# Kernel tuning notes

Measured on AMD Instinct MI355X. Metric: run time of the kernel, lower is better.

The kernel has to match this reference:

```python
import jax, jax.numpy as jnp
import numpy as np

B, S, HID = 2, 2048, 2048
H, KV, D = 16, 4, 128
EPS = 1e-6


def rms_norm(x, w, eps=EPS):
    # Qwen3.5 convention: (1 + weight) * RMSNorm(x), weight init 0
    v = jnp.mean(x * x, axis=-1, keepdims=True)
    return (1.0 + w) * (x * jax.lax.rsqrt(v + eps))


def rotate_half(x):
    x1, x2 = jnp.split(x, 2, axis=-1)
    return jnp.concatenate([-x2, x1], axis=-1)


def apply_rope(x, cos, sin):
    # x: [B,S,h,D]; cos/sin: [S,D]
    c = cos[None, :, None, :]
    s = sin[None, :, None, :]
    return x * c + rotate_half(x) * s


def setup_inputs():
    key = jax.random.key(0)
    ks = jax.random.split(key, 8)
    sc = 0.02
    hidden_states = jax.random.normal(ks[0], (B, S, HID), jnp.float32)
    past_key_value = jnp.zeros((B, 2, KV, S, D), jnp.float32)
    pos = jnp.arange(S, dtype=jnp.float32)
    inv_freq = 1.0 / (10000.0 ** (jnp.arange(0, D, 2, dtype=jnp.float32) / D))
    ang = pos[:, None] * inv_freq[None, :]                    # [S, D/2]
    cos = jnp.concatenate([jnp.cos(ang), jnp.cos(ang)], -1)   # [S, D]
    sin = jnp.concatenate([jnp.sin(ang), jnp.sin(ang)], -1)
    rope_rotary_cos_sin = jnp.stack([cos, sin], axis=1)       # [S, 2, D]
    context_lengths = jnp.full((B,), S, dtype=jnp.int32)
    kvcache_start_index = jnp.zeros((B,), dtype=jnp.int32)
    Wq = jax.random.normal(ks[1], (HID, H * D * 2), jnp.float32) * sc
    Wk = jax.random.normal(ks[2], (HID, KV * D), jnp.float32) * sc
    Wv = jax.random.normal(ks[3], (HID, KV * D), jnp.float32) * sc
    Wo = jax.random.normal(ks[4], (H * D, HID), jnp.float32) * sc
    q_norm_w = jax.random.normal(ks[5], (D,), jnp.float32) * sc
    k_norm_w = jax.random.normal(ks[6], (D,), jnp.float32) * sc
    return {"hidden_states": hidden_states, "past_key_value": past_key_value,
            "rope_rotary_cos_sin": rope_rotary_cos_sin,
            "context_lengths": context_lengths,
            "kvcache_start_index": kvcache_start_index,
            "Wq": Wq, "Wk": Wk, "Wv": Wv, "Wo": Wo,
            "q_norm_w": q_norm_w, "k_norm_w": k_norm_w}


def reference(hidden_states, past_key_value, rope_rotary_cos_sin,
              context_lengths, kvcache_start_index,
              Wq, Wk, Wv, Wo, q_norm_w, k_norm_w):
    # projections
    q_out = jnp.einsum('bsc,cd->bsd', hidden_states, Wq).reshape(B, S, H, 2 * D)
    query, gate = jnp.split(q_out, 2, axis=-1)                # each [B,S,H,D]
    k = jnp.einsum('bsc,cd->bsd', hidden_states, Wk).reshape(B, S, KV, D)
    v = jnp.einsum('bsc,cd->bsd', hidden_states, Wv).reshape(B, S, KV, D)
    # per-head QK RMSNorm
    query = rms_norm(query, q_norm_w)
    k = rms_norm(k, k_norm_w)
    # RoPE
    cos, sin = rope_rotary_cos_sin[:, 0, :], rope_rotary_cos_sin[:, 1, :]
    query = apply_rope(query, cos, sin)
    k = apply_rope(k, cos, sin)
    # write KV cache (prefill at start index 0)
    present = past_key_value.at[:, 0, :, :S, :].set(jnp.transpose(k, (0, 2, 1, 3)))
    present = present.at[:, 1, :, :S, :].set(jnp.transpose(v, (0, 2, 1, 3)))
    # GQA causal attention
    group = H // KV
    k_r = jnp.repeat(k, group, axis=2)                        # [B,S,H,D]
    v_r = jnp.repeat(v, group, axis=2)
    scores = jnp.einsum('bqhd,bkhd->bhqk', query, k_r) / jnp.sqrt(jnp.float32(D))
    causal = jnp.tril(jnp.ones((S, S), dtype=bool))
    scores = jnp.where(causal[None, None], scores, jnp.float32(-1e30))
    probs = jax.nn.softmax(scores, axis=-1)
    attn = jnp.einsum('bhqk,bkhd->bqhd', probs, v_r)          # [B,S,H,D]
    # sigmoid gating + output proj
    attn = attn * jax.nn.sigmoid(gate)
    out = jnp.einsum('bsd,dc->bsc', attn.reshape(B, S, H * D), Wo)
    return out, present
```

## Files before the change

kernel.cpp:

```cpp
#include <hip/hip_runtime.h>
#include <hip/hip_bf16.h>
#include <cstdint>
#include <cstddef>

#define BB   2
#define SS   2048
#define HIDD 2048
#define HH   16
#define KVH  4
#define DD   128
#define NQKV 5120
#define MM   4096

typedef unsigned short u16t;
typedef __attribute__((ext_vector_type(8))) short s16x8;
typedef __attribute__((ext_vector_type(4))) short s16x4;
typedef __attribute__((ext_vector_type(4))) float f32x4;

__device__ __forceinline__ u16t f2bf(float f) {
  unsigned u = __float_as_uint(f);
  u += 0x7fffu + ((u >> 16) & 1u);
  return (u16t)(u >> 16);
}
__device__ __forceinline__ float bf2f(u16t h) {
  return __uint_as_float(((unsigned)h) << 16);
}
__device__ __forceinline__ void gload_lds16(const void* g, void* l) {
  __builtin_amdgcn_global_load_lds(
      (const __attribute__((address_space(1))) unsigned int*)g,
      (__attribute__((address_space(3))) unsigned int*)l, 16, 0, 0);
}
__device__ __forceinline__ unsigned cvtpk_bf16(float lo, float hi) {
  unsigned r;
  asm("v_cvt_pk_bf16_f32 %0, %1, %2" : "=v"(r) : "v"(lo), "v"(hi));
  return r;
}
__device__ __forceinline__ f32x4 fmax4(f32x4 a, f32x4 b) {
  f32x4 r;
  r[0] = fmaxf(a[0], b[0]); r[1] = fmaxf(a[1], b[1]);
  r[2] = fmaxf(a[2], b[2]); r[3] = fmaxf(a[3], b[3]);
  return r;
}

__global__ __launch_bounds__(256) void cast_x(const float* __restrict__ in,
                                              u16t* __restrict__ out) {
  size_t i = ((size_t)blockIdx.x * 256 + threadIdx.x) * 4;
  f32x4 v = *(const f32x4*)(in + i);
  s16x4 o;
  o[0] = (short)f2bf(v[0]); o[1] = (short)f2bf(v[1]);
  o[2] = (short)f2bf(v[2]); o[3] = (short)f2bf(v[3]);
  *(s16x4*)(out + i) = o;
}

__global__ __launch_bounds__(256) void transpose_cast(const float* __restrict__ src,
                                                      u16t* __restrict__ dst, int N) {
  __shared__ float lds[64 * 65];
  int t = threadIdx.x;
  const int ktiles = HIDD / 64;
  int n0 = (blockIdx.x / ktiles) << 6;
  int k0 = (blockIdx.x % ktiles) << 6;
#pragma unroll
  for (int i = 0; i < 16; i++) {
    int idx = i * 256 + t;
    int r = idx >> 6, c = idx & 63;
    lds[c * 65 + r] = src[(size_t)(k0 + r) * N + n0 + c];
  }
  __syncthreads();
#pragma unroll
  for (int i = 0; i < 16; i++) {
    int idx = i * 256 + t;
    int rr = idx >> 6, kk = idx & 63;
    dst[(size_t)(n0 + rr) * HIDD + k0 + kk] = f2bf(lds[rr * 65 + kk]);
  }
}

__device__ __forceinline__ s16x8 ldsfrag(const char* half, int r, int g) {
  return *(const s16x8*)(half + r * 64 + ((g ^ ((r >> 1) & 3)) << 4));
}
__device__ __forceinline__ void stage_half(char* ldsbase, const u16t* gbase,
                                           int K, int kcol, int tid) {
#pragma unroll
  for (int i = 0; i < 2; i++) {
    int o16 = i * 512 + tid;
    int r = o16 >> 2;
    int cs = (o16 & 3) ^ ((r >> 1) & 3);
    gload_lds16(gbase + (size_t)r * K + kcol + cs * 8, ldsbase + o16 * 16);
  }
}

template <typename CT>
__global__ __launch_bounds__(512, 2) void gemm8(const u16t* __restrict__ A,
                                                const u16t* __restrict__ Bt,
                                                CT* __restrict__ C,
                                                int M, int N, int K) {
  extern __shared__ __align__(16) char lds[];
  char* As = lds;
  char* Bs = lds + 65536;
  int tid = threadIdx.x, lane = tid & 63, w = tid >> 6;
  int wm = w >> 2, wn = w & 3;
  int cpx = gridDim.x >> 3;
  int wgid = (blockIdx.x & 7) * cpx + (blockIdx.x >> 3);
  int bm = wgid & 15, bn = wgid >> 4;
  int m0 = bm << 8, n0 = bn << 8;
  const u16t* Ag = A + (size_t)m0 * K;
  const u16t* Bg = Bt + (size_t)n0 * K;
  const int NT = K >> 6;

  stage_half(As, Ag, K, 0, tid);
  stage_half(Bs, Bg, K, 0, tid);
  stage_half(As + 16384, Ag, K, 32, tid);
  stage_half(Bs + 16384, Bg, K, 32, tid);
  stage_half(As + 32768, Ag, K, 64, tid);
  stage_half(Bs + 32768, Bg, K, 64, tid);
  asm volatile("s_waitcnt vmcnt(8)" ::: "memory");
  __builtin_amdgcn_s_barrier();

  const f32x4 fz = {0.f, 0.f, 0.f, 0.f};
  f32x4 acc[8][4];
#pragma unroll
  for (int i = 0; i < 8; i++)
#pragma unroll
    for (int j = 0; j < 4; j++) acc[i][j] = fz;
  s16x8 afr[4], bfr[4];
  int g = lane >> 4;
  int rA = (lane & 15) + wm * 128;
  int rB = (lane & 15) + wn * 64;

  for (int kt = 0; kt < NT; kt++) {
    int cur = kt & 1;
    char* Acur = As + cur * 32768;
    char* Bcur = Bs + cur * 32768;
    char* Anxt = As + (cur ^ 1) * 32768;
    char* Bnxt = Bs + (cur ^ 1) * 32768;
#pragma unroll
    for (int ni = 0; ni < 4; ni++) bfr[ni] = ldsfrag(Bcur, rB + ni * 16, g);
#pragma unroll
    for (int mi = 0; mi < 4; mi++) afr[mi] = ldsfrag(Acur, rA + mi * 16, g);
    if (kt + 1 < NT) stage_half(Anxt + 16384, Ag, K, (kt + 1) * 64 + 32, tid);
    __builtin_amdgcn_s_barrier();
    asm volatile("s_waitcnt lgkmcnt(0)" ::: "memory");
    __builtin_amdgcn_s_setprio(1);
#pragma unroll
    for (int mi = 0; mi < 4; mi++)
#pragma unroll
      for (int ni = 0; ni < 4; ni++)
        acc[mi][ni] = __builtin_amdgcn_mfma_f32_16x16x32_bf16(afr[mi], bfr[ni], acc[mi][ni], 0, 0, 0);
    __builtin_amdgcn_s_setprio(0);
    __builtin_amdgcn_s_barrier();
#pragma unroll
    for (int mi = 0; mi < 4; mi++) afr[mi] = ldsfrag(Acur, rA + 64 + mi * 16, g);
    if (kt + 1 < NT) stage_half(Bnxt + 16384, Bg, K, (kt + 1) * 64 + 32, tid);
    __builtin_amdgcn_s_barrier();
    asm volatile("s_waitcnt lgkmcnt(0)" ::: "memory");
    __builtin_amdgcn_s_setprio(1);
#pragma unroll
    for (int mi = 0; mi < 4; mi++)
#pragma unroll
      for (int ni = 0; ni < 4; ni++)
        acc[4 + mi][ni] = __builtin_amdgcn_mfma_f32_16x16x32_bf16(afr[mi], bfr[ni], acc[4 + mi][ni], 0, 0, 0);
    __builtin_amdgcn_s_setprio(0);
    if (kt + 1 < NT) asm volatile("s_waitcnt vmcnt(8)" ::: "memory");
    else             asm volatile("s_waitcnt vmcnt(0)" ::: "memory");
    __builtin_amdgcn_s_barrier();
#pragma unroll
    for (int ni = 0; ni < 4; ni++) bfr[ni] = ldsfrag(Bcur + 16384, rB + ni * 16, g);
#pragma unroll
    for (int mi = 0; mi < 4; mi++) afr[mi] = ldsfrag(Acur + 16384, rA + mi * 16, g);
    if (kt + 2 < NT) stage_half(Acur, Ag, K, (kt + 2) * 64, tid);
    __builtin_amdgcn_s_barrier();
    asm volatile("s_waitcnt lgkmcnt(0)" ::: "memory");
    __builtin_amdgcn_s_setprio(1);
#pragma unroll
    for (int mi = 0; mi < 4; mi++)
#pragma unroll
      for (int ni = 0; ni < 4; ni++)
        acc[mi][ni] = __builtin_amdgcn_mfma_f32_16x16x32_bf16(afr[mi], bfr[ni], acc[mi][ni], 0, 0, 0);
    __builtin_amdgcn_s_setprio(0);
    __builtin_amdgcn_s_barrier();
#pragma unroll
    for (int mi = 0; mi < 4; mi++) afr[mi] = ldsfrag(Acur + 16384, rA + 64 + mi * 16, g);
    if (kt + 2 < NT) stage_half(Bcur, Bg, K, (kt + 2) * 64, tid);
    __builtin_amdgcn_s_barrier();
    asm volatile("s_waitcnt lgkmcnt(0)" ::: "memory");
    __builtin_amdgcn_s_setprio(1);
#pragma unroll
    for (int mi = 0; mi < 4; mi++)
#pragma unroll
      for (int ni = 0; ni < 4; ni++)
        acc[4 + mi][ni] = __builtin_amdgcn_mfma_f32_16x16x32_bf16(afr[mi], bfr[ni], acc[4 + mi][ni], 0, 0, 0);
    __builtin_amdgcn_s_setprio(0);
    if (kt < NT - 1) {
      if (kt + 2 < NT) asm volatile("s_waitcnt vmcnt(8)" ::: "memory");
      else             asm volatile("s_waitcnt vmcnt(4)" ::: "memory");
    }
    __builtin_amdgcn_s_barrier();
  }
#pragma unroll
  for (int mi = 0; mi < 8; mi++)
#pragma unroll
    for (int ni = 0; ni < 4; ni++) {
      int row0 = m0 + wm * 128 + mi * 16 + ((lane >> 4) << 2);
      int col = n0 + wn * 64 + ni * 16 + (lane & 15);
#pragma unroll
      for (int j = 0; j < 4; j++) {
        if constexpr (sizeof(CT) == 2)
          C[(size_t)(row0 + j) * N + col] = f2bf(acc[mi][ni][j]);
        else
          C[(size_t)(row0 + j) * N + col] = acc[mi][ni][j];
      }
    }
}

template <typename CT>
__global__ __launch_bounds__(256) void gemm_bt(const u16t* __restrict__ A,
                                               const u16t* __restrict__ Bt,
                                               CT* __restrict__ C,
                                               int M, int N, int K) {
  __shared__ __align__(16) char As[128 * 64];
  __shared__ __align__(16) char Bs[128 * 64];
  int tid = threadIdx.x;
  int lane = tid & 63;
  int w = tid >> 6;
  int cpx = gridDim.x >> 3;
  int wgid = ((int)blockIdx.x & 7) * cpx + ((int)blockIdx.x >> 3);
  int mtiles = M >> 7;
  int bm = wgid % mtiles;
  int bn = wgid / mtiles;
  int m0 = bm << 7, n0 = bn << 7;
  int wr = (w >> 1) * 64, wc = (w & 1) * 64;

  const f32x4 fz = {0.f, 0.f, 0.f, 0.f};
  f32x4 acc[4][4];
#pragma unroll
  for (int i = 0; i < 4; i++)
#pragma unroll
    for (int j = 0; j < 4; j++) acc[i][j] = fz;

  for (int k0 = 0; k0 < K; k0 += 32) {
    __syncthreads();
#pragma unroll
    for (int i = 0; i < 2; i++) {
      int idx = i * 256 + tid;
      int r = idx >> 2, c = idx & 3;
      int csrc = c ^ ((r >> 1) & 3);
      gload_lds16(A + (size_t)(m0 + r) * K + k0 + csrc * 8, As + idx * 16);
      gload_lds16(Bt + (size_t)(n0 + r) * K + k0 + csrc * 8, Bs + idx * 16);
    }
    __syncthreads();
    s16x8 af[4], bf[4];
    int g = lane >> 4;
#pragma unroll
    for (int mi = 0; mi < 4; mi++) {
      int r = wr + mi * 16 + (lane & 15);
      af[mi] = *(const s16x8*)(As + r * 64 + ((g ^ ((r >> 1) & 3)) << 4));
    }
#pragma unroll
    for (int ni = 0; ni < 4; ni++) {
      int r = wc + ni * 16 + (lane & 15);
      bf[ni] = *(const s16x8*)(Bs + r * 64 + ((g ^ ((r >> 1) & 3)) << 4));
    }
#pragma unroll
    for (int mi = 0; mi < 4; mi++)
#pragma unroll
      for (int ni = 0; ni < 4; ni++)
        acc[mi][ni] = __builtin_amdgcn_mfma_f32_16x16x32_bf16(af[mi], bf[ni], acc[mi][ni], 0, 0, 0);
  }
#pragma unroll
  for (int mi = 0; mi < 4; mi++)
#pragma unroll
    for (int ni = 0; ni < 4; ni++) {
      int row0 = m0 + wr + mi * 16 + ((lane >> 4) << 2);
      int col = n0 + wc + ni * 16 + (lane & 15);
#pragma unroll
      for (int j = 0; j < 4; j++) {
        if constexpr (sizeof(CT) == 2)
          C[(size_t)(row0 + j) * N + col] = f2bf(acc[mi][ni][j]);
        else
          C[(size_t)(row0 + j) * N + col] = acc[mi][ni][j];
      }
    }
}

__global__ __launch_bounds__(256) void qk_norm_rope(const u16t* __restrict__ Cqkv,
                                                    const float* __restrict__ rope,
                                                    const float* __restrict__ qw,
                                                    const float* __restrict__ kw,
                                                    u16t* __restrict__ Qb,
                                                    u16t* __restrict__ Kb,
                                                    u16t* __restrict__ Gs,
                                                    float* __restrict__ present) {
  int wid = blockIdx.x * 4 + (threadIdx.x >> 6);
  int lane = threadIdx.x & 63;
  const int NQ = BB * SS * HH;
  if (wid < NQ) {
    int b = wid >> 15;
    int rem = wid & 32767;
    int s = rem >> 4, h = rem & 15;
    const u16t* base = Cqkv + (size_t)(b * SS + s) * NQKV + h * 256;
    float xlo = bf2f(base[lane]), xhi = bf2f(base[64 + lane]);
    float ss = xlo * xlo + xhi * xhi;
    ss += __shfl_xor(ss, 1);  ss += __shfl_xor(ss, 2);  ss += __shfl_xor(ss, 4);
    ss += __shfl_xor(ss, 8);  ss += __shfl_xor(ss, 16); ss += __shfl_xor(ss, 32);
    float r = rsqrtf(ss * (1.f / 128.f) + 1e-6f);
    float qlo = xlo * r * (1.f + qw[lane]);
    float qhi = xhi * r * (1.f + qw[64 + lane]);
    const float* cs = rope + (size_t)s * 256;
    float clo = cs[lane], chi = cs[64 + lane];
    float slo = cs[128 + lane], shi = cs[192 + lane];
    const float SC = 0.08838834764831845f * 1.4426950408889634f;
    float olo = (qlo * clo - qhi * slo) * SC;
    float ohi = (qhi * chi + qlo * shi) * SC;
    size_t qoff = (((size_t)b * HH + h) * SS + s) * DD;
    Qb[qoff + lane] = f2bf(olo);
    Qb[qoff + 64 + lane] = f2bf(ohi);
    float glo = bf2f(base[128 + lane]), ghi = bf2f(base[192 + lane]);
    size_t goff = ((size_t)(b * SS + s)) * (HH * DD) + h * DD;
    Gs[goff + lane] = f2bf(1.f / (1.f + __expf(-glo)));
    Gs[goff + 64 + lane] = f2bf(1.f / (1.f + __expf(-ghi)));
  } else {
    int wid2 = wid - NQ;
    int b = wid2 >> 13;
    int rem = wid2 & 8191;
    int s = rem >> 2, kv = rem & 3;
    const u16t* base = Cqkv + (size_t)(b * SS + s) * NQKV + 4096 + kv * 128;
    float xlo = bf2f(base[lane]), xhi = bf2f(base[64 + lane]);
    float ss = xlo * xlo + xhi * xhi;
    ss += __shfl_xor(ss, 1);  ss += __shfl_xor(ss, 2);  ss += __shfl_xor(ss, 4);
    ss += __shfl_xor(ss, 8);  ss += __shfl_xor(ss, 16); ss += __shfl_xor(ss, 32);
    float r = rsqrtf(ss * (1.f / 128.f) + 1e-6f);
    float klo = xlo * r * (1.f + kw[lane]);
    float khi = xhi * r * (1.f + kw[64 + lane]);
    const float* cs = rope + (size_t)s * 256;
    float clo = cs[lane], chi = cs[64 + lane];
    float slo = cs[128 + lane], shi = cs[192 + lane];
    float olo = klo * clo - khi * slo;
    float ohi = khi * chi + klo * shi;
    size_t koff = (((size_t)b * KVH + kv) * SS + s) * DD;
    Kb[koff + lane] = f2bf(olo);
    Kb[koff + 64 + lane] = f2bf(ohi);
    size_t poff = (((size_t)(b * 2 * KVH + kv)) * SS + s) * DD;
    present[poff + lane] = olo;
    present[poff + 64 + lane] = ohi;
  }
}

__global__ __launch_bounds__(256) void v_write(const u16t* __restrict__ Cqkv,
                                               float* __restrict__ present,
                                               u16t* __restrict__ Vtb) {
  __shared__ float lds[128 * 65];
  int t = threadIdx.x;
  int b = blockIdx.x >> 7;
  int kv = (blockIdx.x >> 5) & 3;
  int s0 = (blockIdx.x & 31) << 6;
#pragma unroll
  for (int i = 0; i < 32; i++) {
    int idx = i * 256 + t;
    int sp = idx >> 7, d = idx & 127;
    float v = bf2f(Cqkv[(size_t)(b * SS + s0 + sp) * NQKV + 4608 + kv * 128 + d]);
    present[(((size_t)(b * 2 * KVH + KVH + kv)) * SS + s0 + sp) * DD + d] = v;
    lds[d * 65 + sp] = v;
  }
  __syncthreads();
#pragma unroll
  for (int i = 0; i < 8; i++) {
    int d = i * 16 + (t >> 4);
    int sp = (t & 15) * 4;
    s16x4 pk;
    pk[0] = (short)f2bf(lds[d * 65 + sp + 0]);
    pk[1] = (short)f2bf(lds[d * 65 + sp + 1]);
    pk[2] = (short)f2bf(lds[d * 65 + sp + 2]);
    pk[3] = (short)f2bf(lds[d * 65 + sp + 3]);
    *(s16x4*)(Vtb + ((size_t)(b * KVH + kv) * DD + d) * SS + s0 + sp) = pk;
  }
}

__global__ __launch_bounds__(256) void attn_kernel(const u16t* __restrict__ Qb,
                                                   const u16t* __restrict__ Kb,
                                                   const u16t* __restrict__ Vtb,
                                                   const u16t* __restrict__ Gs,
                                                   u16t* __restrict__ AttG) {
  __shared__ __align__(16) char Ks[2][16384];
  __shared__ __align__(16) char Vs[2][16384];
  __shared__ __align__(16) char Ps[4 * 2048];

  int tid = threadIdx.x, lane = tid & 63, w = tid >> 6;
  int x = blockIdx.x & 7;
  int b = x >> 2, kv = x & 3;
  int rr = blockIdx.x >> 3;
  int h = kv * 4 + (rr & 3);
  int p = rr >> 2;

  const u16t* Kbase = Kb + (((size_t)(b * KVH + kv)) * SS) * DD;
  const u16t* Vbase = Vtb + (((size_t)(b * KVH + kv)) * DD) * SS;

  auto stageK = [&](int kt, int buf) {
#pragma unroll
    for (int i = 0; i < 4; i++) {
      int idx = i * 256 + tid;
      int r_ = idx >> 4, c_ = idx & 15;
      gload_lds16(Kbase + (size_t)(kt * 64 + r_) * DD + (c_ ^ (r_ & 7)) * 8, Ks[buf] + idx * 16);
    }
  };
  auto stageV = [&](int kt, int buf) {
#pragma unroll
    for (int i = 0; i < 4; i++) {
      int idx = i * 256 + tid;
      int r_ = idx >> 3, c_ = idx & 7;
      gload_lds16(Vbase + (size_t)r_ * SS + kt * 64 + (c_ ^ (r_ & 7)) * 8, Vs[buf] + idx * 16);
    }
  };

  const f32x4 fz = {0.f, 0.f, 0.f, 0.f};
  int g = lane >> 4;
  int q15 = lane & 15;
  int q7 = q15 & 7;
  char* pq = Ps + w * 2048 + q15 * 128;
  int cur = 0;

  stageK(0, 0);
  stageV(0, 0);

  for (int seg = 0; seg < 2; seg++) {
    int qt = (seg == 0) ? (31 - p) : p;
    const u16t* Qbase = Qb + (((size_t)(b * HH + h)) * SS + qt * 64) * DD;
    s16x8 qf[4];
    {
      const u16t* qrow = Qbase + (size_t)(w * 16 + q15) * DD + g * 8;
#pragma unroll
      for (int ks = 0; ks < 4; ks++) qf[ks] = *(const s16x8*)(qrow + ks * 32);
    }
    f32x4 acco[8];
#pragma unroll
    for (int f = 0; f < 8; f++) acco[f] = fz;
    float mrun = -INFINITY, lrun = 0.f;

    if (seg == 0) {
      asm volatile("s_waitcnt vmcnt(0)" ::: "memory");
      __builtin_amdgcn_s_barrier();
    }

    for (int kt = 0; kt <= qt; kt++) {
      bool havenext = (kt < qt) || (seg == 0);
      if (havenext) {
        int nk = (kt < qt) ? (kt + 1) : 0;
        stageK(nk, cur ^ 1);
        stageV(nk, cur ^ 1);
      }
      f32x4 accs[4];
#pragma unroll
      for (int ni = 0; ni < 4; ni++) accs[ni] = fz;
#pragma unroll
      for (int ni = 0; ni < 4; ni++) {
        int r = ni * 16 + q15;
#pragma unroll
        for (int ks = 0; ks < 4; ks++) {
          int g2 = ks * 4 + g;
          s16x8 bfk = *(const s16x8*)(Ks[cur] + r * 256 + ((g2 ^ (r & 7)) << 4));
          accs[ni] = __builtin_amdgcn_mfma_f32_16x16x32_bf16(bfk, qf[ks], accs[ni], 0, 0, 0);
        }
      }
      if (kt == qt) {
        int ql = w * 16 + q15;
#pragma unroll
        for (int ni = 0; ni < 4; ni++)
#pragma unroll
          for (int j = 0; j < 4; j++) {
            int kl = ni * 16 + (g << 2) + j;
            if (kl > ql) accs[ni][j] = -1e30f;
          }
      }
      f32x4 m4 = fmax4(fmax4(accs[0], accs[1]), fmax4(accs[2], accs[3]));
      float mt = fmaxf(fmaxf(m4[0], m4[1]), fmaxf(m4[2], m4[3]));
      mt = fmaxf(mt, __shfl_xor(mt, 16));
      mt = fmaxf(mt, __shfl_xor(mt, 32));
      float mnew = fmaxf(mrun, mt);
      float alpha = __builtin_amdgcn_exp2f(mrun - mnew);
      mrun = mnew;
      float rs = 0.f;
#pragma unroll
      for (int ni = 0; ni < 4; ni++)
#pragma unroll
        for (int j = 0; j < 4; j++) {
          float pv = __builtin_amdgcn_exp2f(accs[ni][j] - mnew);
          accs[ni][j] = pv;
          rs += pv;
        }
      rs += __shfl_xor(rs, 16);
      rs += __shfl_xor(rs, 32);
      lrun = lrun * alpha + rs;
      float ar[4];
#pragma unroll
      for (int j = 0; j < 4; j++) ar[j] = __shfl(alpha, (g << 2) + j);
#pragma unroll
      for (int f = 0; f < 8; f++)
#pragma unroll
        for (int j = 0; j < 4; j++) acco[f][j] *= ar[j];

#pragma unroll
      for (int ni = 0; ni < 4; ni++)
#pragma unroll
        for (int jj = 0; jj < 2; jj++) {
          unsigned pk32 = cvtpk_bf16(accs[ni][2 * jj], accs[ni][2 * jj + 1]);
          int gr = ni * 2 + (g >> 1);
          int off = ((gr ^ q7) << 4) + ((g & 1) << 3) + (jj << 2);
          *(unsigned*)(pq + off) = pk32;
        }
#pragma unroll
      for (int ks2 = 0; ks2 < 2; ks2++) {
        s16x8 pa = *(const s16x8*)(pq + (((ks2 * 4 + g) ^ q7) << 4));
#pragma unroll
        for (int f = 0; f < 8; f++) {
          int d = f * 16 + q15;
          s16x8 vf = *(const s16x8*)(Vs[cur] + d * 128 + (((ks2 * 4 + g) ^ (d & 7)) << 4));
          acco[f] = __builtin_amdgcn_mfma_f32_16x16x32_bf16(pa, vf, acco[f], 0, 0, 0);
        }
      }
      if (havenext) {
        asm volatile("s_waitcnt vmcnt(0)" ::: "memory");
        __builtin_amdgcn_s_barrier();
        cur ^= 1;
      }
    }
    float lr[4];
#pragma unroll
    for (int j = 0; j < 4; j++) lr[j] = __shfl(lrun, (g << 2) + j);
#pragma unroll
    for (int f = 0; f < 8; f++) {
      int d = f * 16 + q15;
#pragma unroll
      for (int j = 0; j < 4; j++) {
        int srow = qt * 64 + w * 16 + (g << 2) + j;
        float o = acco[f][j] / lr[j];
        size_t off = ((size_t)b * SS + srow) * (HH * DD) + h * DD + d;
        float gt = bf2f(Gs[off]);
        AttG[off] = f2bf(o * gt);
      }
    }
  }
}

extern "C" void kernel_launch(void* const* d_in, const int* in_sizes, int n_in,
                              void* d_out, int out_size, void* d_ws, size_t ws_size,
                              hipStream_t stream) {
  const float* hidden = (const float*)d_in[0];
  const float* rope   = (const float*)d_in[2];
  const float* Wq     = (const float*)d_in[5];
  const float* Wk     = (const float*)d_in[6];
  const float* Wv     = (const float*)d_in[7];
  const float* Wo     = (const float*)d_in[8];
  const float* qw     = (const float*)d_in[9];
  const float* kw     = (const float*)d_in[10];
  float* out = (float*)d_out;
  float* present = out + (size_t)BB * SS * HIDD;

  char* ws = (char*)d_ws;
  u16t* Xb    = (u16t*)(ws);
  u16t* Wt    = (u16t*)(ws + 16777216);
  u16t* Wot   = (u16t*)(ws + 37748736);
  u16t* Cqkv  = (u16t*)(ws + 46137344);
  u16t* Qb    = (u16t*)(ws + 88080384);
  u16t* Kb    = (u16t*)(ws + 104857600);
  u16t* Vtb   = (u16t*)(ws + 109051904);
  u16t* Gs    = (u16t*)(ws + 113246208);
  u16t* AttG  = Xb;

  (void)hipFuncSetAttribute(reinterpret_cast<const void*>(gemm8<u16t>),
                            hipFuncAttributeMaxDynamicSharedMemorySize, 131072);

  cast_x<<<8192, 256, 0, stream>>>(hidden, Xb);
  transpose_cast<<<(4096 / 64) * 32, 256, 0, stream>>>(Wq, Wt, 4096);
  transpose_cast<<<(512 / 64) * 32, 256, 0, stream>>>(Wk, Wt + (size_t)4096 * HIDD, 512);
  transpose_cast<<<(512 / 64) * 32, 256, 0, stream>>>(Wv, Wt + (size_t)4608 * HIDD, 512);
  transpose_cast<<<(2048 / 64) * 32, 256, 0, stream>>>(Wo, Wot, 2048);
  gemm8<u16t><<<(MM / 256) * (4096 / 256), 512, 131072, stream>>>(Xb, Wt, Cqkv, MM, NQKV, HIDD);
  gemm_bt<u16t><<<(MM / 128) * (1024 / 128), 256, 0, stream>>>(
      Xb, Wt + (size_t)4096 * HIDD, Cqkv + 4096, MM, NQKV, HIDD);
  qk_norm_rope<<<(BB * SS * (HH + KVH)) / 4, 256, 0, stream>>>(Cqkv, rope, qw, kw, Qb, Kb, Gs, present);
  v_write<<<BB * KVH * (SS / 64), 256, 0, stream>>>(Cqkv, present, Vtb);
  attn_kernel<<<BB * HH * (SS / 128), 256, 0, stream>>>(Qb, Kb, Vtb, Gs, AttG);
  gemm_bt<float><<<(MM / 128) * (HIDD / 128), 256, 0, stream>>>(AttG, Wot, out, MM, HIDD, HIDD);
}
```

Before: 291.9 us.

## Fuse prep kernels, use gemm8 for output projection, tidy softmax packing

Merges the input cast and the four weight transpose-casts into one prep_all launch, cutting the launch count and letting those small kernels overlap. Switches the output projection from the 128-tile gemm_bt to the 256-tile, 512-thread gemm8 with float output, which gives more reuse per block but only 128 blocks. In attention, the row sum now uses a vector-add tree and the P tile is written to LDS as 64-bit stores instead of 32-bit ones. The output GEMM change carries the main risk, because 128 blocks may leave part of the GPU idle.

```diff
diff --git a/kernel.cpp b/kernel.cpp
--- a/kernel.cpp
+++ b/kernel.cpp
@@ -42,23 +42,35 @@
   return r;
 }
 
-__global__ __launch_bounds__(256) void cast_x(const float* __restrict__ in,
-                                              u16t* __restrict__ out) {
-  size_t i = ((size_t)blockIdx.x * 256 + threadIdx.x) * 4;
-  f32x4 v = *(const f32x4*)(in + i);
-  s16x4 o;
-  o[0] = (short)f2bf(v[0]); o[1] = (short)f2bf(v[1]);
-  o[2] = (short)f2bf(v[2]); o[3] = (short)f2bf(v[3]);
-  *(s16x4*)(out + i) = o;
-}
-
-__global__ __launch_bounds__(256) void transpose_cast(const float* __restrict__ src,
-                                                      u16t* __restrict__ dst, int N) {
+__global__ __launch_bounds__(256) void prep_all(const float* __restrict__ hidden,
+                                                const float* __restrict__ Wq,
+                                                const float* __restrict__ Wk,
+                                                const float* __restrict__ Wv,
+                                                const float* __restrict__ Wo,
+                                                u16t* __restrict__ Xb,
+                                                u16t* __restrict__ Wt,
+                                                u16t* __restrict__ Wot) {
   __shared__ float lds[64 * 65];
+  int bid = blockIdx.x;
   int t = threadIdx.x;
+  if (bid < 8192) {
+    size_t i = ((size_t)bid * 256 + t) * 4;
+    f32x4 v = *(const f32x4*)(hidden + i);
+    s16x4 o;
+    o[0] = (short)f2bf(v[0]); o[1] = (short)f2bf(v[1]);
+    o[2] = (short)f2bf(v[2]); o[3] = (short)f2bf(v[3]);
+    *(s16x4*)(Xb + i) = o;
+    return;
+  }
+  bid -= 8192;
+  const float* src; u16t* dst; int N;
+  if (bid < 2048)      { src = Wq; dst = Wt;                         N = 4096; }
+  else if (bid < 2304) { src = Wk; dst = Wt + (size_t)4096 * HIDD;   N = 512;  bid -= 2048; }
+  else if (bid < 2560) { src = Wv; dst = Wt + (size_t)4608 * HIDD;   N = 512;  bid -= 2304; }
+  else                 { src = Wo; dst = Wot;                        N = 2048; bid -= 2560; }
   const int ktiles = HIDD / 64;
-  int n0 = (blockIdx.x / ktiles) << 6;
-  int k0 = (blockIdx.x % ktiles) << 6;
+  int n0 = (bid / ktiles) << 6;
+  int k0 = (bid % ktiles) << 6;
 #pragma unroll
   for (int i = 0; i < 16; i++) {
     int idx = i * 256 + t;
@@ -476,15 +488,15 @@
       float mnew = fmaxf(mrun, mt);
       float alpha = __builtin_amdgcn_exp2f(mrun - mnew);
       mrun = mnew;
-      float rs = 0.f;
 #pragma unroll
       for (int ni = 0; ni < 4; ni++)
 #pragma unroll
-        for (int j = 0; j < 4; j++) {
-          float pv = __builtin_amdgcn_exp2f(accs[ni][j] - mnew);
-          accs[ni][j] = pv;
-          rs += pv;
-        }
+        for (int j = 0; j < 4; j++)
+          accs[ni][j] = __builtin_amdgcn_exp2f(accs[ni][j] - mnew);
+      f32x4 s01 = accs[0] + accs[1];
+      f32x4 s23 = accs[2] + accs[3];
+      f32x4 s4 = s01 + s23;
+      float rs = (s4[0] + s4[1]) + (s4[2] + s4[3]);
       rs += __shfl_xor(rs, 16);
       rs += __shfl_xor(rs, 32);
       lrun = lrun * alpha + rs;
@@ -497,14 +509,13 @@
         for (int j = 0; j < 4; j++) acco[f][j] *= ar[j];
 
 #pragma unroll
-      for (int ni = 0; ni < 4; ni++)
-#pragma unroll
-        for (int jj = 0; jj < 2; jj++) {
-          unsigned pk32 = cvtpk_bf16(accs[ni][2 * jj], accs[ni][2 * jj + 1]);
-          int gr = ni * 2 + (g >> 1);
-          int off = ((gr ^ q7) << 4) + ((g & 1) << 3) + (jj << 2);
-          *(unsigned*)(pq + off) = pk32;
-        }
+      for (int ni = 0; ni < 4; ni++) {
+        uint2 pk;
+        pk.x = cvtpk_bf16(accs[ni][0], accs[ni][1]);
+        pk.y = cvtpk_bf16(accs[ni][2], accs[ni][3]);
+        int gr = ni * 2 + (g >> 1);
+        *(uint2*)(pq + ((gr ^ q7) << 4) + ((g & 1) << 3)) = pk;
+      }
 #pragma unroll
       for (int ks2 = 0; ks2 < 2; ks2++) {
         s16x8 pa = *(const s16x8*)(pq + (((ks2 * 4 + g) ^ q7) << 4));
@@ -566,17 +577,15 @@
 
   (void)hipFuncSetAttribute(reinterpret_cast<const void*>(gemm8<u16t>),
                             hipFuncAttributeMaxDynamicSharedMemorySize, 131072);
-
-  cast_x<<<8192, 256, 0, stream>>>(hidden, Xb);
-  transpose_cast<<<(4096 / 64) * 32, 256, 0, stream>>>(Wq, Wt, 4096);
-  transpose_cast<<<(512 / 64) * 32, 256, 0, stream>>>(Wk, Wt + (size_t)4096 * HIDD, 512);
-  transpose_cast<<<(512 / 64) * 32, 256, 0, stream>>>(Wv, Wt + (size_t)4608 * HIDD, 512);
-  transpose_cast<<<(2048 / 64) * 32, 256, 0, stream>>>(Wo, Wot, 2048);
+  (void)hipFuncSetAttribute(reinterpret_cast<const void*>(gemm8<float>),
+                            hipFuncAttributeMaxDynamicSharedMemorySize, 131072);
+
+  prep_all<<<8192 + 3584, 256, 0, stream>>>(hidden, Wq, Wk, Wv, Wo, Xb, Wt, Wot);
   gemm8<u16t><<<(MM / 256) * (4096 / 256), 512, 131072, stream>>>(Xb, Wt, Cqkv, MM, NQKV, HIDD);
   gemm_bt<u16t><<<(MM / 128) * (1024 / 128), 256, 0, stream>>>(
       Xb, Wt + (size_t)4096 * HIDD, Cqkv + 4096, MM, NQKV, HIDD);
   qk_norm_rope<<<(BB * SS * (HH + KVH)) / 4, 256, 0, stream>>>(Cqkv, rope, qw, kw, Qb, Kb, Gs, present);
   v_write<<<BB * KVH * (SS / 64), 256, 0, stream>>>(Cqkv, present, Vtb);
   attn_kernel<<<BB * HH * (SS / 128), 256, 0, stream>>>(Qb, Kb, Vtb, Gs, AttG);
-  gemm_bt<float><<<(MM / 128) * (HIDD / 128), 256, 0, stream>>>(AttG, Wot, out, MM, HIDD, HIDD);
-}
+  gemm8<float><<<(MM / 256) * (HIDD / 256), 512, 131072, stream>>>(AttG, Wot, out, MM, HIDD, HIDD);
+}
```

New measurement: 289.0 us. About the same (-1.0%).
